# Optimization experiments

Measured on AMD Instinct MI355X. Metric: run time of the kernel, lower is better.

## Reference

```python
import jax, jax.numpy as jnp
import numpy as np
import math

IN_CH = 32
OUT_CH = 32
NODE_NUM = 24
BATCH = 32768
# skeleton edges: self-loops + chain (parent -> child), matching init_kwargs
_SRC = list(range(24)) + list(range(23))
_DST = list(range(24)) + list(range(1, 24))


def _build_mask():
    # block mask: block (dst, src) of size [OUT_CH, IN_CH] set to 1 per edge
    m = np.zeros((OUT_CH * NODE_NUM, IN_CH * NODE_NUM), dtype=np.float32)
    for s, d in zip(_SRC, _DST):
        m[OUT_CH * d:OUT_CH * (d + 1), IN_CH * s:IN_CH * (s + 1)] = 1.0
    return jnp.asarray(m)


def setup_inputs() -> dict:
    key = jax.random.key(0)
    kx, kw, kb = jax.random.split(key, 3)
    mask = _build_mask()
    dim = IN_CH * NODE_NUM
    # kaiming-uniform-like per-block init approximated by scaled normal; only
    # values inside mask blocks matter (forward multiplies by mask anyway)
    weight = jax.random.normal(kw, (OUT_CH * NODE_NUM, dim), dtype=jnp.float32) * (1.0 / math.sqrt(IN_CH))
    bound = 1.0 / math.sqrt(dim)
    bias = jax.random.uniform(kb, (OUT_CH * NODE_NUM,), dtype=jnp.float32, minval=-bound, maxval=bound)
    x = jax.random.normal(kx, (BATCH, dim), dtype=jnp.float32)
    return {"x": x, "weight": weight, "bias": bias, "mask": mask}


def reference(x, weight, bias, mask):
    # F.linear(x, weight * mask, bias) == x @ (weight*mask)^T + bias
    w = weight * mask
    return jnp.einsum("bi,oi->bo", x, w) + bias
```

## Files before the change

kernel.cpp:

```cpp
#include <hip/hip_runtime.h>
#include <hip/hip_bf16.h>


typedef __bf16 bf16x4 __attribute__((ext_vector_type(4)));
typedef __bf16 bf16x8 __attribute__((ext_vector_type(8)));
typedef float  f32x4  __attribute__((ext_vector_type(4)));

#define DIM 768
#define M_TILE 32
#define LDS_STRIDE 776

__global__ __launch_bounds__(256, 3)
void skeleton_linear_kernel(const float* __restrict__ x,
                            const float* __restrict__ w,
                            const float* __restrict__ bias,
                            float* __restrict__ out)
{
    __shared__ __bf16 xs[M_TILE * LDS_STRIDE];

    const int tid = threadIdx.x;
    const long row0 = (long)blockIdx.x * M_TILE;

    {
        const float4* gx = (const float4*)(x + row0 * DIM);
#pragma unroll
        for (int g = 0; g < 3; ++g) {
            float4 st[8];
#pragma unroll
            for (int i = 0; i < 8; ++i) st[i] = gx[tid + 256 * (8 * g + i)];
#pragma unroll
            for (int i = 0; i < 8; ++i) {
                int f = tid + 256 * (8 * g + i);
                int r = f / 192;
                int c4 = f % 192;
                bf16x4 v;
                v[0] = (__bf16)st[i].x; v[1] = (__bf16)st[i].y;
                v[2] = (__bf16)st[i].z; v[3] = (__bf16)st[i].w;
                *(bf16x4*)(&xs[r * LDS_STRIDE + c4 * 4]) = v;
            }
        }
    }
    __syncthreads();

    const int lane = tid & 63;
    const int wave = tid >> 6;
    const int quad = lane >> 4;
    const int l16  = lane & 15;

    for (int i = 0; i < 6; ++i) {
        const int d  = wave * 6 + i;
        const int kb = (d == 0) ? 0 : 32 * (d - 1);
        const int nk = (d == 0) ? 1 : 2;

        f32x4 acc[2][2];
#pragma unroll
        for (int mi = 0; mi < 2; ++mi)
#pragma unroll
            for (int ni = 0; ni < 2; ++ni)
#pragma unroll
                for (int r = 0; r < 4; ++r) acc[mi][ni][r] = 0.f;

        for (int kt = 0; kt < nk; ++kt) {
            const int k0 = kb + 32 * kt + 8 * quad;
            bf16x8 a[2];
#pragma unroll
            for (int mi = 0; mi < 2; ++mi)
                a[mi] = *(const bf16x8*)&xs[(16 * mi + l16) * LDS_STRIDE + k0];
            bf16x8 b[2];
#pragma unroll
            for (int ni = 0; ni < 2; ++ni) {
                const float* wr = w + (long)(32 * d + 16 * ni + l16) * DIM + k0;
                float4 w0 = *(const float4*)wr;
                float4 w1 = *(const float4*)(wr + 4);
                bf16x8 bb;
                bb[0] = (__bf16)w0.x; bb[1] = (__bf16)w0.y;
                bb[2] = (__bf16)w0.z; bb[3] = (__bf16)w0.w;
                bb[4] = (__bf16)w1.x; bb[5] = (__bf16)w1.y;
                bb[6] = (__bf16)w1.z; bb[7] = (__bf16)w1.w;
                b[ni] = bb;
            }
#pragma unroll
            for (int mi = 0; mi < 2; ++mi)
#pragma unroll
                for (int ni = 0; ni < 2; ++ni)
                    acc[mi][ni] = __builtin_amdgcn_mfma_f32_16x16x32_bf16(
                        a[mi], b[ni], acc[mi][ni], 0, 0, 0);
        }

#pragma unroll
        for (int ni = 0; ni < 2; ++ni) {
            const float bi = bias[32 * d + 16 * ni + l16];
#pragma unroll
            for (int mi = 0; mi < 2; ++mi) {
                const long ob = (row0 + 16 * mi + 4 * quad) * DIM
                              + 32 * d + 16 * ni + l16;
#pragma unroll
                for (int r = 0; r < 4; ++r)
                    out[ob + (long)r * DIM] = acc[mi][ni][r] + bi;
            }
        }
    }
}

extern "C" void kernel_launch(void* const* d_in, const int* in_sizes, int n_in,
                              void* d_out, int out_size, void* d_ws, size_t ws_size,
                              hipStream_t stream) {
    const float* x    = (const float*)d_in[0];
    const float* w    = (const float*)d_in[1];
    const float* bias = (const float*)d_in[2];
    float* out = (float*)d_out;

    const int BATCH = 32768;
    dim3 grid(BATCH / M_TILE);
    skeleton_linear_kernel<<<grid, 256, 0, stream>>>(x, w, bias, out);
}
```

Baseline: 201.3 us.

## Load x directly from global into MFMA operands, drop LDS staging, halve row tile

Removes the shared-memory staging of the x tile. Each lane now reads its fp32 x fragment straight from global memory, converts it to bf16 in registers and feeds it to the MFMA. The row tile shrinks from 32 to 16, which doubles the grid, and the occupancy hint rises to 4 blocks. This eliminates the LDS writes, the LDS reads and the block barrier. In exchange, each x element is read from global by several waves that overlap in k-range, and the W rows are re-read per block twice as often. The k-loop is fully unrolled, with a skip for node 0.

```diff
diff --git a/kernel.cpp b/kernel.cpp
--- a/kernel.cpp
+++ b/kernel.cpp
@@ -2,102 +2,60 @@
 #include <hip/hip_bf16.h>
 
 
-typedef __bf16 bf16x4 __attribute__((ext_vector_type(4)));
 typedef __bf16 bf16x8 __attribute__((ext_vector_type(8)));
 typedef float  f32x4  __attribute__((ext_vector_type(4)));
 
 #define DIM 768
-#define M_TILE 32
-#define LDS_STRIDE 776
 
-__global__ __launch_bounds__(256, 3)
+__device__ __forceinline__ bf16x8 cvt8(const float* __restrict__ p) {
+    float4 lo = *(const float4*)p;
+    float4 hi = *(const float4*)(p + 4);
+    bf16x8 r;
+    r[0] = (__bf16)lo.x; r[1] = (__bf16)lo.y; r[2] = (__bf16)lo.z; r[3] = (__bf16)lo.w;
+    r[4] = (__bf16)hi.x; r[5] = (__bf16)hi.y; r[6] = (__bf16)hi.z; r[7] = (__bf16)hi.w;
+    return r;
+}
+
+__global__ __launch_bounds__(256, 4)
 void skeleton_linear_kernel(const float* __restrict__ x,
                             const float* __restrict__ w,
                             const float* __restrict__ bias,
                             float* __restrict__ out)
 {
-    __shared__ __bf16 xs[M_TILE * LDS_STRIDE];
-
-    const int tid = threadIdx.x;
-    const long row0 = (long)blockIdx.x * M_TILE;
-
-    {
-        const float4* gx = (const float4*)(x + row0 * DIM);
-#pragma unroll
-        for (int g = 0; g < 3; ++g) {
-            float4 st[8];
-#pragma unroll
-            for (int i = 0; i < 8; ++i) st[i] = gx[tid + 256 * (8 * g + i)];
-#pragma unroll
-            for (int i = 0; i < 8; ++i) {
-                int f = tid + 256 * (8 * g + i);
-                int r = f / 192;
-                int c4 = f % 192;
-                bf16x4 v;
-                v[0] = (__bf16)st[i].x; v[1] = (__bf16)st[i].y;
-                v[2] = (__bf16)st[i].z; v[3] = (__bf16)st[i].w;
-                *(bf16x4*)(&xs[r * LDS_STRIDE + c4 * 4]) = v;
-            }
-        }
-    }
-    __syncthreads();
-
+    const int tid  = threadIdx.x;
     const int lane = tid & 63;
     const int wave = tid >> 6;
     const int quad = lane >> 4;
     const int l16  = lane & 15;
 
+    const long row0 = (long)blockIdx.x * 16;
+    const float* xrow = x + (row0 + l16) * DIM;
+
+#pragma unroll
     for (int i = 0; i < 6; ++i) {
         const int d  = wave * 6 + i;
-        const int kb = (d == 0) ? 0 : 32 * (d - 1);
-        const int nk = (d == 0) ? 1 : 2;
+        const int kb = 32 * d - 32;
 
-        f32x4 acc[2][2];
+        f32x4 acc0 = {0.f, 0.f, 0.f, 0.f};
+        f32x4 acc1 = {0.f, 0.f, 0.f, 0.f};
+
 #pragma unroll
-        for (int mi = 0; mi < 2; ++mi)
-#pragma unroll
-            for (int ni = 0; ni < 2; ++ni)
-#pragma unroll
-                for (int r = 0; r < 4; ++r) acc[mi][ni][r] = 0.f;
-
-        for (int kt = 0; kt < nk; ++kt) {
+        for (int kt = 0; kt < 2; ++kt) {
+            if (d == 0 && kt == 0) continue;
             const int k0 = kb + 32 * kt + 8 * quad;
-            bf16x8 a[2];
-#pragma unroll
-            for (int mi = 0; mi < 2; ++mi)
-                a[mi] = *(const bf16x8*)&xs[(16 * mi + l16) * LDS_STRIDE + k0];
-            bf16x8 b[2];
-#pragma unroll
-            for (int ni = 0; ni < 2; ++ni) {
-                const float* wr = w + (long)(32 * d + 16 * ni + l16) * DIM + k0;
-                float4 w0 = *(const float4*)wr;
-                float4 w1 = *(const float4*)(wr + 4);
-                bf16x8 bb;
-                bb[0] = (__bf16)w0.x; bb[1] = (__bf16)w0.y;
-                bb[2] = (__bf16)w0.z; bb[3] = (__bf16)w0.w;
-                bb[4] = (__bf16)w1.x; bb[5] = (__bf16)w1.y;
-                bb[6] = (__bf16)w1.z; bb[7] = (__bf16)w1.w;
-                b[ni] = bb;
-            }
-#pragma unroll
-            for (int mi = 0; mi < 2; ++mi)
-#pragma unroll
-                for (int ni = 0; ni < 2; ++ni)
-                    acc[mi][ni] = __builtin_amdgcn_mfma_f32_16x16x32_bf16(
-                        a[mi], b[ni], acc[mi][ni], 0, 0, 0);
+            bf16x8 a = cvt8(xrow + k0);
+            const float* w0 = w + (long)(32 * d + l16) * DIM + k0;
+            acc0 = __builtin_amdgcn_mfma_f32_16x16x32_bf16(a, cvt8(w0), acc0, 0, 0, 0);
+            acc1 = __builtin_amdgcn_mfma_f32_16x16x32_bf16(a, cvt8(w0 + 16 * DIM), acc1, 0, 0, 0);
         }
 
+        const float bi0 = bias[32 * d + l16];
+        const float bi1 = bias[32 * d + 16 + l16];
+        float* o = out + (row0 + 4 * quad) * DIM + 32 * d + l16;
 #pragma unroll
-        for (int ni = 0; ni < 2; ++ni) {
-            const float bi = bias[32 * d + 16 * ni + l16];
-#pragma unroll
-            for (int mi = 0; mi < 2; ++mi) {
-                const long ob = (row0 + 16 * mi + 4 * quad) * DIM
-                              + 32 * d + 16 * ni + l16;
-#pragma unroll
-                for (int r = 0; r < 4; ++r)
-                    out[ob + (long)r * DIM] = acc[mi][ni][r] + bi;
-            }
+        for (int r = 0; r < 4; ++r) {
+            o[(long)r * DIM]      = acc0[r] + bi0;
+            o[(long)r * DIM + 16] = acc1[r] + bi1;
         }
     }
 }
@@ -111,6 +69,6 @@
     float* out = (float*)d_out;
 
     const int BATCH = 32768;
-    dim3 grid(BATCH / M_TILE);
+    dim3 grid(BATCH / 16);
     skeleton_linear_kernel<<<grid, 256, 0, stream>>>(x, w, bias, out);
 }
```

Measured after the change: 232.4 us. 15.5% more time.
